# Performance work log

Hardware: AMD Instinct MI355X
Metric: run time of the kernel (lower is better)

The kernel has to match this reference:

```python
import jax, jax.numpy as jnp
import numpy as np

B, D1, N, F_IN, F_OUT = 8, 16, 2048, 64, 64


def setup_inputs() -> dict:
    key = jax.random.key(0)
    k1, k2, k3 = jax.random.split(key, 3)
    x = jax.random.normal(k1, (B, D1, N, F_IN), dtype=jnp.float32)
    adj = jax.random.uniform(k2, (B, N, N), dtype=jnp.float32)
    weight = jax.random.normal(k3, (F_IN, F_OUT), dtype=jnp.float32) * (1.0 / np.sqrt(F_IN))
    return {"x": x, "adj": adj, "weight": weight}


def reference(x, adj, weight):
    # x: [B, D1, N, F_in], adj: [B, N, N], weight: [F_in, F_out]
    # Original: per (b, i) loops -> support = x[b,i] @ W; out[b,i] = adj[b] @ support
    # Fused as batched einsums. Note: the module's bias parameter is unused in forward.
    support = jnp.einsum('binf,fg->bing', x, weight)          # feature transform
    out = jnp.einsum('bnm,bimg->bing', adj, support)           # adjacency aggregation
    return out
```

## Files before the change

kernel.cpp:

```cpp
#include <hip/hip_runtime.h>
#include <hip/hip_bf16.h>

typedef __attribute__((ext_vector_type(8))) short bf16x8;
typedef __attribute__((ext_vector_type(4))) float f32x4;

#define NB    8
#define ND1   16
#define NN    2048
#define NF    64
#define GN    1024

__device__ static inline ushort f2bf(float f) {
    unsigned int u = __builtin_bit_cast(unsigned int, f);
    unsigned int r = (u + 0x7FFFu + ((u >> 16) & 1u)) >> 16;
    return (ushort)r;
}

__device__ static inline void gload_lds16(const void* g, void* l) {
    __builtin_amdgcn_global_load_lds(
        (const __attribute__((address_space(1))) void*)g,
        (__attribute__((address_space(3))) void*)l, 16, 0, 0);
}

__global__ __launch_bounds__(256) void conv_adj_kernel(
    const float* __restrict__ adj, ushort* __restrict__ adjb, int n4)
{
    int idx = blockIdx.x * blockDim.x + threadIdx.x;
    int stride = gridDim.x * blockDim.x;
    const float4* a4 = (const float4*)adj;
    ushort4* o4 = (ushort4*)adjb;
    for (int i = idx; i < n4; i += stride) {
        float4 v = a4[i];
        ushort4 r;
        r.x = f2bf(v.x); r.y = f2bf(v.y); r.z = f2bf(v.z); r.w = f2bf(v.w);
        o4[i] = r;
    }
}

__global__ __launch_bounds__(256) void support_kernel(
    const float* __restrict__ x, const float* __restrict__ w,
    ushort* __restrict__ sT)
{
    __shared__ __align__(16) float Ws[64 * 64];
    __shared__ __align__(16) float xs[64 * 65];
    __shared__ __align__(16) ushort tr[64 * 72];

    int t = threadIdx.x;
    int bid = blockIdx.x;
    int b  = bid >> 9;
    int r  = bid & 511;
    int i  = r >> 5;
    int mb = r & 31;

    const float4* w4 = (const float4*)w;
    const float4* x4 = (const float4*)(x + (((size_t)(b * ND1 + i)) * NN + mb * 64) * NF);
#pragma unroll
    for (int j = 0; j < 4; ++j) {
        float4 wv = w4[j * 256 + t];
        int fl = j * 1024 + t * 4;
        Ws[fl + 0] = wv.x; Ws[fl + 1] = wv.y; Ws[fl + 2] = wv.z; Ws[fl + 3] = wv.w;
        float4 xv = x4[j * 256 + t];
        int ml = fl >> 6, f = fl & 63;
        float* xr = &xs[ml * 65 + f];
        xr[0] = xv.x; xr[1] = xv.y; xr[2] = xv.z; xr[3] = xv.w;
    }
    __syncthreads();

    int ml = t & 63;
    int g0 = (t >> 6) * 16;
    f32x4 acc4[4] = {0.f, 0.f, 0.f, 0.f};
    for (int f = 0; f < 64; ++f) {
        float xv = xs[ml * 65 + f];
        const f32x4* wp = (const f32x4*)&Ws[f * 64 + g0];
#pragma unroll
        for (int q = 0; q < 4; ++q) acc4[q] += xv * wp[q];
    }
#pragma unroll
    for (int j = 0; j < 16; ++j)
        tr[(g0 + j) * 72 + ml] = f2bf(acc4[j >> 2][j & 3]);
    __syncthreads();

    int g = t >> 2, part = t & 3;
    const uint4* src = (const uint4*)&tr[g * 72 + part * 16];
    uint4* dst = (uint4*)(sT + ((size_t)(b * GN + i * 64 + g)) * NN + mb * 64 + part * 16);
    dst[0] = src[0];
    dst[1] = src[1];
}

template <bool PRECONV>
__global__ __launch_bounds__(256) void gcn_gemm_kernel(
    const ushort* __restrict__ adjb,
    const float* __restrict__ adjf,
    const ushort* __restrict__ sT,
    float* __restrict__ out)
{
    __shared__ __align__(16) ushort lA[128 * 64];
    __shared__ __align__(16) ushort lB[128 * 64];

    int t = threadIdx.x;

    int bid0 = blockIdx.x;
    int bid = (bid0 & 7) * 128 + (bid0 >> 3);

    int b  = bid >> 7;
    int rr = bid & 127;
    int mt = rr >> 3;
    int nt = rr & 7;
    int n0 = mt * 128;
    int c0 = nt * 128;

    const ushort* Ab = adjb + (size_t)b * NN * NN;
    const float*  Af = adjf + (size_t)b * NN * NN;
    const ushort* Bb = sT + (size_t)b * GN * NN;

    int lane = t & 63, wv = t >> 6;
    int wr = (wv >> 1) * 64, wc = (wv & 1) * 64;

    f32x4 acc[4][4];
#pragma unroll
    for (int a = 0; a < 4; ++a)
#pragma unroll
        for (int c = 0; c < 4; ++c) acc[a][c] = (f32x4){0.f, 0.f, 0.f, 0.f};

    int sRow = t >> 3;
    int sCol = (t & 7) * 8;

    for (int k0 = 0; k0 < NN; k0 += 64) {
        if (PRECONV) {
#pragma unroll
            for (int i = 0; i < 4; ++i)
                gload_lds16(Ab + (size_t)(n0 + i * 32 + sRow) * NN + k0 + sCol,
                            &lA[(i * 32 + sRow) * 64 + sCol]);
        } else {
#pragma unroll
            for (int i = 0; i < 4; ++i) {
                const float* src = Af + (size_t)(n0 + i * 32 + sRow) * NN + k0 + sCol;
                float4 v0 = *(const float4*)src;
                float4 v1 = *(const float4*)(src + 4);
                union { bf16x8 v; ushort u[8]; } p;
                p.u[0] = f2bf(v0.x); p.u[1] = f2bf(v0.y);
                p.u[2] = f2bf(v0.z); p.u[3] = f2bf(v0.w);
                p.u[4] = f2bf(v1.x); p.u[5] = f2bf(v1.y);
                p.u[6] = f2bf(v1.z); p.u[7] = f2bf(v1.w);
                *(bf16x8*)&lA[(i * 32 + sRow) * 64 + sCol] = p.v;
            }
        }
#pragma unroll
        for (int i = 0; i < 4; ++i)
            gload_lds16(Bb + (size_t)(c0 + i * 32 + sRow) * NN + k0 + sCol,
                        &lB[(i * 32 + sRow) * 64 + sCol]);

        __syncthreads();

#pragma unroll
        for (int kk = 0; kk < 2; ++kk) {
            bf16x8 af[4], bfr[4];
#pragma unroll
            for (int a = 0; a < 4; ++a)
                af[a] = *(const bf16x8*)&lA[(wr + a * 16 + (lane & 15)) * 64 + kk * 32 + (lane >> 4) * 8];
#pragma unroll
            for (int c = 0; c < 4; ++c)
                bfr[c] = *(const bf16x8*)&lB[(wc + c * 16 + (lane & 15)) * 64 + kk * 32 + (lane >> 4) * 8];
#pragma unroll
            for (int a = 0; a < 4; ++a)
#pragma unroll
                for (int c = 0; c < 4; ++c)
                    acc[a][c] = __builtin_amdgcn_mfma_f32_16x16x32_bf16(af[a], bfr[c], acc[a][c], 0, 0, 0);
        }
        __syncthreads();
    }

#pragma unroll
    for (int a = 0; a < 4; ++a) {
        int row0 = n0 + wr + a * 16 + (lane >> 4) * 4;
#pragma unroll
        for (int c = 0; c < 4; ++c) {
            int col = c0 + wc + c * 16 + (lane & 15);
            int ii = col >> 6, g = col & 63;
            float* op = out + (((size_t)(b * ND1 + ii)) * NN + row0) * NF + g;
#pragma unroll
            for (int e = 0; e < 4; ++e)
                op[e * NF] = acc[a][c][e];
        }
    }
}

extern "C" void kernel_launch(void* const* d_in, const int* in_sizes, int n_in,
                              void* d_out, int out_size, void* d_ws, size_t ws_size,
                              hipStream_t stream) {
    const float* x   = (const float*)d_in[0];
    const float* adj = (const float*)d_in[1];
    const float* w   = (const float*)d_in[2];
    float* out = (float*)d_out;

    ushort* sT   = (ushort*)d_ws;
    ushort* adjb = (ushort*)((char*)d_ws + 33554432);
    bool preconv = ws_size >= (size_t)100663296;

    support_kernel<<<dim3(NB * ND1 * (NN / 64)), dim3(256), 0, stream>>>(x, w, sT);

    if (preconv) {
        conv_adj_kernel<<<dim3(2048), dim3(256), 0, stream>>>(adj, adjb, NB * NN * NN / 4);
        gcn_gemm_kernel<true><<<dim3(NB * 16 * 8), dim3(256), 0, stream>>>(adjb, nullptr, sT, out);
    } else {
        gcn_gemm_kernel<false><<<dim3(NB * 16 * 8), dim3(256), 0, stream>>>(nullptr, adj, sT, out);
    }
}
```

Before: 376.1 us.

## Replace preconverted GEMM with 256x256-tile, 8-wave, triple-buffered pipelined kernel

```diff
diff --git a/kernel.cpp b/kernel.cpp
--- a/kernel.cpp
+++ b/kernel.cpp
@@ -87,29 +87,132 @@
     dst[1] = src[1];
 }
 
-template <bool PRECONV>
-__global__ __launch_bounds__(256) void gcn_gemm_kernel(
+__global__ __launch_bounds__(512, 2) void gemm8_kernel(
     const ushort* __restrict__ adjb,
-    const float* __restrict__ adjf,
     const ushort* __restrict__ sT,
+    float* __restrict__ out)
+{
+    __shared__ __align__(16) ushort lds[3 * 16384];
+
+    const int t    = threadIdx.x;
+    const int lane = t & 63;
+    const int w    = t >> 6;
+    const int wm   = w >> 2;
+    const int wn   = w & 3;
+
+    int bid  = blockIdx.x;
+    int tile = (bid & 7) * 32 + (bid >> 3);
+    int b    = tile >> 5;
+    int r    = tile & 31;
+    int n0   = (r >> 2) * 256;
+    int c0   = (r & 3) * 256;
+
+    const ushort* Ab = adjb + (size_t)b * NN * NN + (size_t)n0 * NN;
+    const ushort* Bb = sT   + (size_t)b * GN * NN + (size_t)c0 * NN;
+
+    const int rS  = lane & 15;
+    const int cgS = lane >> 4;
+    const int fq  = ((lane >> 4) * 16 + (lane & 15)) * 8;
+
+    f32x4 acc[8][4];
+#pragma unroll
+    for (int a = 0; a < 8; ++a)
+#pragma unroll
+        for (int c = 0; c < 4; ++c) acc[a][c] = (f32x4){0.f, 0.f, 0.f, 0.f};
+
+    auto stageA = [&](int kt, int q) {
+#pragma unroll
+        for (int j = 0; j < 2; ++j) {
+            int stripe = j * 8 + w;
+            gload_lds16(Ab + (size_t)(stripe * 16 + rS) * NN + kt * 32 + cgS * 8,
+                        &lds[q * 16384 + j * 4096 + w * 512 + lane * 8]);
+        }
+    };
+    auto stageB = [&](int kt, int q) {
+#pragma unroll
+        for (int j = 0; j < 2; ++j) {
+            int stripe = j * 8 + w;
+            gload_lds16(Bb + (size_t)(stripe * 16 + rS) * NN + kt * 32 + cgS * 8,
+                        &lds[q * 16384 + 8192 + j * 4096 + w * 512 + lane * 8]);
+        }
+    };
+
+    stageA(0, 0); stageB(0, 0);
+    stageA(1, 1); stageB(1, 1);
+
+    int q = 0, qn = 2;
+    for (int kt = 0; kt < 64; ++kt) {
+        if (kt < 63) asm volatile("s_waitcnt vmcnt(4)" ::: "memory");
+        else         asm volatile("s_waitcnt vmcnt(0)" ::: "memory");
+        asm volatile("s_barrier" ::: "memory");
+
+        const ushort* La = &lds[q * 16384];
+        const ushort* Lb = &lds[q * 16384 + 8192];
+
+        bf16x8 af[4], bfr[4];
+#pragma unroll
+        for (int a = 0; a < 4; ++a)
+            af[a] = *(const bf16x8*)&La[(wm * 8 + a) * 512 + fq];
+#pragma unroll
+        for (int c = 0; c < 4; ++c)
+            bfr[c] = *(const bf16x8*)&Lb[(wn * 4 + c) * 512 + fq];
+        if (kt < 62) stageA(kt + 2, qn);
+        asm volatile("s_barrier" ::: "memory");
+        __builtin_amdgcn_s_setprio(1);
+#pragma unroll
+        for (int a = 0; a < 4; ++a)
+#pragma unroll
+            for (int c = 0; c < 4; ++c)
+                acc[a][c] = __builtin_amdgcn_mfma_f32_16x16x32_bf16(af[a], bfr[c], acc[a][c], 0, 0, 0);
+        __builtin_amdgcn_s_setprio(0);
+
+#pragma unroll
+        for (int a = 0; a < 4; ++a)
+            af[a] = *(const bf16x8*)&La[(wm * 8 + 4 + a) * 512 + fq];
+        if (kt < 62) stageB(kt + 2, qn);
+        asm volatile("s_barrier" ::: "memory");
+        __builtin_amdgcn_s_setprio(1);
+#pragma unroll
+        for (int a = 0; a < 4; ++a)
+#pragma unroll
+            for (int c = 0; c < 4; ++c)
+                acc[4 + a][c] = __builtin_amdgcn_mfma_f32_16x16x32_bf16(af[a], bfr[c], acc[4 + a][c], 0, 0, 0);
+        __builtin_amdgcn_s_setprio(0);
+
+        q  = (q  == 2) ? 0 : q  + 1;
+        qn = (qn == 2) ? 0 : qn + 1;
+    }
+
+#pragma unroll
+    for (int a = 0; a < 8; ++a) {
+        int row0 = n0 + wm * 128 + a * 16 + (lane >> 4) * 4;
+#pragma unroll
+        for (int c = 0; c < 4; ++c) {
+            int col = c0 + wn * 64 + c * 16 + (lane & 15);
+            int ii = col >> 6, g = col & 63;
+            float* op = out + (((size_t)(b * ND1 + ii)) * NN + row0) * NF + g;
+#pragma unroll
+            for (int e = 0; e < 4; ++e)
+                op[e * NF] = acc[a][c][e];
+        }
+    }
+}
+
+__global__ __launch_bounds__(256) void gcn_gemm_fb_kernel(
+    const float* __restrict__ adjf, const ushort* __restrict__ sT,
     float* __restrict__ out)
 {
     __shared__ __align__(16) ushort lA[128 * 64];
     __shared__ __align__(16) ushort lB[128 * 64];
 
     int t = threadIdx.x;
-
     int bid0 = blockIdx.x;
     int bid = (bid0 & 7) * 128 + (bid0 >> 3);
-
     int b  = bid >> 7;
     int rr = bid & 127;
-    int mt = rr >> 3;
-    int nt = rr & 7;
-    int n0 = mt * 128;
-    int c0 = nt * 128;
-
-    const ushort* Ab = adjb + (size_t)b * NN * NN;
+    int n0 = (rr >> 3) * 128;
+    int c0 = (rr & 7) * 128;
+
     const float*  Af = adjf + (size_t)b * NN * NN;
     const ushort* Bb = sT + (size_t)b * GN * NN;
 
@@ -126,32 +229,23 @@
     int sCol = (t & 7) * 8;
 
     for (int k0 = 0; k0 < NN; k0 += 64) {
-        if (PRECONV) {
-#pragma unroll
-            for (int i = 0; i < 4; ++i)
-                gload_lds16(Ab + (size_t)(n0 + i * 32 + sRow) * NN + k0 + sCol,
-                            &lA[(i * 32 + sRow) * 64 + sCol]);
-        } else {
-#pragma unroll
-            for (int i = 0; i < 4; ++i) {
-                const float* src = Af + (size_t)(n0 + i * 32 + sRow) * NN + k0 + sCol;
-                float4 v0 = *(const float4*)src;
-                float4 v1 = *(const float4*)(src + 4);
-                union { bf16x8 v; ushort u[8]; } p;
-                p.u[0] = f2bf(v0.x); p.u[1] = f2bf(v0.y);
-                p.u[2] = f2bf(v0.z); p.u[3] = f2bf(v0.w);
-                p.u[4] = f2bf(v1.x); p.u[5] = f2bf(v1.y);
-                p.u[6] = f2bf(v1.z); p.u[7] = f2bf(v1.w);
-                *(bf16x8*)&lA[(i * 32 + sRow) * 64 + sCol] = p.v;
-            }
+#pragma unroll
+        for (int i = 0; i < 4; ++i) {
+            const float* src = Af + (size_t)(n0 + i * 32 + sRow) * NN + k0 + sCol;
+            float4 v0 = *(const float4*)src;
+            float4 v1 = *(const float4*)(src + 4);
+            union { bf16x8 v; ushort u[8]; } p;
+            p.u[0] = f2bf(v0.x); p.u[1] = f2bf(v0.y);
+            p.u[2] = f2bf(v0.z); p.u[3] = f2bf(v0.w);
+            p.u[4] = f2bf(v1.x); p.u[5] = f2bf(v1.y);
+            p.u[6] = f2bf(v1.z); p.u[7] = f2bf(v1.w);
+            *(bf16x8*)&lA[(i * 32 + sRow) * 64 + sCol] = p.v;
         }
 #pragma unroll
         for (int i = 0; i < 4; ++i)
             gload_lds16(Bb + (size_t)(c0 + i * 32 + sRow) * NN + k0 + sCol,
                         &lB[(i * 32 + sRow) * 64 + sCol]);
-
         __syncthreads();
-
 #pragma unroll
         for (int kk = 0; kk < 2; ++kk) {
             bf16x8 af[4], bfr[4];
@@ -169,7 +263,6 @@
         }
         __syncthreads();
     }
-
 #pragma unroll
     for (int a = 0; a < 4; ++a) {
         int row0 = n0 + wr + a * 16 + (lane >> 4) * 4;
@@ -201,8 +294,8 @@
 
     if (preconv) {
         conv_adj_kernel<<<dim3(2048), dim3(256), 0, stream>>>(adj, adjb, NB * NN * NN / 4);
-        gcn_gemm_kernel<true><<<dim3(NB * 16 * 8), dim3(256), 0, stream>>>(adjb, nullptr, sT, out);
+        gemm8_kernel<<<dim3(256), dim3(512), 0, stream>>>(adjb, sT, out);
     } else {
-        gcn_gemm_kernel<false><<<dim3(NB * 16 * 8), dim3(256), 0, stream>>>(nullptr, adj, sT, out);
-    }
-}
+        gcn_gemm_fb_kernel<<<dim3(NB * 16 * 8), dim3(256), 0, stream>>>(adj, sT, out);
+    }
+}
```

Measured after the change: 341.0 us. 1.1x faster.
